# Optimization experiments

Hardware: AMD Instinct MI355X
Metric: run time of the kernel (lower is better)

## Reference

```python
import jax, jax.numpy as jnp
import numpy as np

H = 256          # hidden_dim
K = 5            # num_mixtures
Z = 32           # latent_dim
A = 3            # action dim
B, T = 128, 512
IN = Z + A       # LSTM input features
MDN = K * (1 + 2 * Z)  # 325


def setup_inputs() -> dict:
    key = jax.random.key(0)
    ks = jax.random.split(key, 8)
    s_in = 1.0 / np.sqrt(IN)
    s_h = 1.0 / np.sqrt(H)
    return {
        "z_t": jax.random.normal(ks[0], (B, T, Z), jnp.float32),
        "a_t": jax.random.normal(ks[1], (B, T, A), jnp.float32),
        # LSTM params: fused gate kernels, gate order [i, f, g, o]
        "Wx": jax.random.normal(ks[2], (IN, 4 * H), jnp.float32) * s_in,
        "Wh": jax.random.normal(ks[3], (H, 4 * H), jnp.float32) * s_h,
        "b": jnp.zeros((4 * H,), jnp.float32),
        # MDN head Dense(325)
        "Wd": jax.random.normal(ks[4], (H, MDN), jnp.float32) * s_h,
        "bd": jnp.zeros((MDN,), jnp.float32),
    }


def _mdnrnn(z_t, a_t, Wx, Wh, b, Wd, bd):
    x = jnp.concatenate([z_t, a_t], axis=-1)          # (B,T,IN)
    # hoist the input projection out of the recurrence (same math)
    xproj = jnp.einsum("bti,ig->btg", x, Wx)          # (B,T,4H)
    xproj_t = jnp.swapaxes(xproj, 0, 1)               # (T,B,4H)
    bsz = x.shape[0]
    c0 = jnp.zeros((bsz, H), x.dtype)
    h0 = jnp.zeros((bsz, H), x.dtype)

    def step(carry, xp):
        c, h = carry
        gates = xp + h @ Wh + b                        # (B,4H)
        i, f, g, o = jnp.split(gates, 4, axis=-1)
        i = jax.nn.sigmoid(i)
        f = jax.nn.sigmoid(f)
        g = jnp.tanh(g)
        o = jax.nn.sigmoid(o)
        c = f * c + i * g
        h = o * jnp.tanh(c)
        return (c, h), h

    final_carry, hs = jax.lax.scan(step, (c0, h0), xproj_t)
    outputs = jnp.swapaxes(hs, 0, 1)                  # (B,T,H)

    mdn = outputs @ Wd + bd                           # (B,T,325)
    log_pi, mu, log_sigma = jnp.split(mdn, [K, K + K * Z * 2 // 2 + K * Z - K], axis=-1)
    # splits: [K, (1+Z)*K] -> log_pi (K), mu (K*Z), log_sigma (K*Z)
    log_pi, mu, log_sigma = mdn[..., :K], mdn[..., K:K + K * Z], mdn[..., K + K * Z:]
    bt = outputs.shape[:2]
    mu = mu.reshape(bt[0], bt[1], K, Z)
    log_sigma = log_sigma.reshape(bt[0], bt[1], K, Z)
    log_pi = jax.nn.log_softmax(log_pi, axis=-1)
    sigma = jnp.exp(log_sigma) + 1e-06
    return log_pi, mu, sigma, final_carry


def reference(z_t, a_t, Wx, Wh, b, Wd, bd):
    return _mdnrnn(z_t, a_t, Wx, Wh, b, Wd, bd)
```

## Files before the change

### kernel.cpp

```cpp
#include <hip/hip_runtime.h>
#include <hip/hip_bf16.h>
#include <math.h>

#define T_LEN 512
#define B_SZ  128
#define H_DIM 256
#define G_DIM 1024
#define IN_D  35
#define MDN_D 325
#define K_MIX 5

#define NSLICE 4
#define BG     2
#define NGRP   64

static constexpr long OFF_MU    = 327680L;
static constexpr long OFF_SIGMA = 10813440L;
static constexpr long OFF_C     = 21299200L;
static constexpr long OFF_H     = 21331968L;

static constexpr size_t WS_OUT = 0;
static constexpr size_t WS_HG  = 33554432;

typedef unsigned uint2v  __attribute__((ext_vector_type(2)));
typedef float    float2v __attribute__((ext_vector_type(2)));
typedef float    float4v __attribute__((ext_vector_type(4)));

__device__ __forceinline__ float fast_sigmoid(float x) { return 1.0f / (1.0f + __expf(-x)); }
__device__ __forceinline__ float fast_tanh(float x) {
    return 1.0f - 2.0f / (__expf(2.0f * x) + 1.0f);
}

__device__ __forceinline__ void pk_fma_lo(float2v& acc, float2v w, float2v h) {
    asm("v_pk_fma_f32 %0, %1, %2, %0 op_sel:[0,0,0] op_sel_hi:[1,0,1]"
        : "+v"(acc) : "v"(w), "v"(h));
}
__device__ __forceinline__ void pk_fma_hi(float2v& acc, float2v w, float2v h) {
    asm("v_pk_fma_f32 %0, %1, %2, %0 op_sel:[0,1,0] op_sel_hi:[1,1,1]"
        : "+v"(acc) : "v"(w), "v"(h));
}

__global__ __launch_bounds__(512, 1) void lstm6_kernel(
    const float* __restrict__ z_t, const float* __restrict__ a_t,
    const float* __restrict__ Wx,  const float* __restrict__ Wh,
    const float* __restrict__ bias,
    float* __restrict__ h_glb,
    __hip_bfloat16* __restrict__ outs,
    float* __restrict__ out_c, float* __restrict__ out_h)
{
    const int bid = blockIdx.x;
    const int gr  = bid & 63;
    const int s   = bid >> 6;
    const int tid = threadIdx.x;
    const int cg  = tid >> 2;
    const int kq  = tid & 3;
    const int lc0 = cg * 2;
    const int gate = lc0 >> 6;
    const int j0   = lc0 & 63;
    const int gcol0 = gate * 256 + s * 64 + j0;

    __shared__ __align__(16) float h_lds[BG][4][68];
    __shared__ __align__(16) float x_lds[BG][44];
    __shared__ __align__(16) float g_red[BG][256];

    for (int i = tid; i < BG * 4 * 68; i += 512) ((float*)h_lds)[i] = 0.0f;
    if (tid < BG * 9) { int b = tid / 9, k = tid - 9 * b; x_lds[b][35 + k] = 0.0f; }

    float2v W2[64];
    #pragma unroll
    for (int i = 0; i < 64; ++i) {
        const size_t r = (size_t)(kq * 64 + i) * G_DIM;
        W2[i].x = Wh[r + gcol0];
        W2[i].y = Wh[r + gcol0 + 1];
    }
    float2v X2[10];
    #pragma unroll
    for (int i = 0; i < 10; ++i) {
        int xk = kq * 10 + i;
        bool ok = (xk < IN_D);
        X2[i].x = ok ? Wx[(size_t)xk * G_DIM + gcol0]     : 0.0f;
        X2[i].y = ok ? Wx[(size_t)xk * G_DIM + gcol0 + 1] : 0.0f;
    }
    #pragma unroll
    for (int i = 0; i < 64; ++i) asm volatile("" : "+v"(W2[i]));
    #pragma unroll
    for (int i = 0; i < 10; ++i) asm volatile("" : "+v"(X2[i]));

    const int cb = tid >> 6;
    const int cj = tid & 63;
    const float bc0 = bias[0 * 256 + s * 64 + cj];
    const float bc1 = bias[1 * 256 + s * 64 + cj];
    const float bc2 = bias[2 * 256 + s * 64 + cj];
    const float bc3 = bias[3 * 256 + s * 64 + cj];
    float c_reg = 0.0f;

    const int q  = tid - 128;
    const int pb = (q >= 96) ? 1 : 0;
    const int pp = q - 96 * pb;
    const int pk0 = pp * 2;
    const int pkk = pk0 + ((pk0 >= s * 64) ? 64 : 0);

    const int batch0 = gr * BG;
    float* hg = h_glb + (size_t)gr * (2 * BG * H_DIM);

    if (tid >= 384 && tid < 448) {
        int qq = tid - 384, b = qq >> 5, k = qq & 31;
        x_lds[b][k] = z_t[((size_t)(batch0 + b) * T_LEN + 0) * 32 + k];
    } else if (tid >= 448 && tid < 448 + BG * 3) {
        int qq = tid - 448, b = (qq >= 3), k = qq - 3 * b;
        x_lds[b][32 + k] = a_t[((size_t)(batch0 + b) * T_LEN + 0) * 3 + k];
    }
    __syncthreads();

    for (int t = 0; t < T_LEN; ++t) {
        if (t > 0 && tid >= 128 && tid < 320) {
            const unsigned want = (unsigned)((t - 1) & 3);
            const float* ap = hg + ((t - 1) & 1) * (BG * H_DIM) + pb * H_DIM + pkk;
            uint2v u;
            do {
                asm volatile("global_load_dwordx2 %0, %1, off sc0 sc1\n\t"
                             "s_waitcnt vmcnt(0)"
                             : "=v"(u) : "v"(ap) : "memory");
            } while ((u.x & 3u) != want || (u.y & 3u) != want);
            float* dst = &h_lds[pb][pkk >> 6][pkk & 63];
            dst[0] = __uint_as_float(u.x);
            dst[1] = __uint_as_float(u.y);
        }
        __syncthreads();

        float2v acc0 = {0.0f, 0.0f}, acc1 = {0.0f, 0.0f};
        {
            const float4v* hp0 = (const float4v*)h_lds[0][kq];
            const float4v* hp1 = (const float4v*)h_lds[1][kq];
            #pragma unroll
            for (int i4 = 0; i4 < 16; ++i4) {
                float4v hv0 = hp0[i4];
                float4v hv1 = hp1[i4];
                float2v h0lo = __builtin_shufflevector(hv0, hv0, 0, 1);
                float2v h0hi = __builtin_shufflevector(hv0, hv0, 2, 3);
                float2v h1lo = __builtin_shufflevector(hv1, hv1, 0, 1);
                float2v h1hi = __builtin_shufflevector(hv1, hv1, 2, 3);
                pk_fma_lo(acc0, W2[4*i4+0], h0lo); pk_fma_lo(acc1, W2[4*i4+0], h1lo);
                pk_fma_hi(acc0, W2[4*i4+1], h0lo); pk_fma_hi(acc1, W2[4*i4+1], h1lo);
                pk_fma_lo(acc0, W2[4*i4+2], h0hi); pk_fma_lo(acc1, W2[4*i4+2], h1hi);
                pk_fma_hi(acc0, W2[4*i4+3], h0hi); pk_fma_hi(acc1, W2[4*i4+3], h1hi);
            }
            #pragma unroll
            for (int i = 0; i < 5; ++i) {
                float2v xv0 = *(const float2v*)&x_lds[0][kq * 10 + 2 * i];
                float2v xv1 = *(const float2v*)&x_lds[1][kq * 10 + 2 * i];
                pk_fma_lo(acc0, X2[2*i],   xv0); pk_fma_lo(acc1, X2[2*i],   xv1);
                pk_fma_hi(acc0, X2[2*i+1], xv0); pk_fma_hi(acc1, X2[2*i+1], xv1);
            }
        }
        float a00 = acc0.x, a01 = acc0.y, a10 = acc1.x, a11 = acc1.y;
        a00 += __shfl_xor(a00, 1, 64); a00 += __shfl_xor(a00, 2, 64);
        a01 += __shfl_xor(a01, 1, 64); a01 += __shfl_xor(a01, 2, 64);
        a10 += __shfl_xor(a10, 1, 64); a10 += __shfl_xor(a10, 2, 64);
        a11 += __shfl_xor(a11, 1, 64); a11 += __shfl_xor(a11, 2, 64);
        if (kq == 0) {
            g_red[0][lc0] = a00; g_red[0][lc0 + 1] = a01;
            g_red[1][lc0] = a10; g_red[1][lc0 + 1] = a11;
        }
        __syncthreads();

        if (tid < 128) {
            float gi = g_red[cb][      cj] + bc0;
            float gf = g_red[cb][ 64 + cj] + bc1;
            float gg = g_red[cb][128 + cj] + bc2;
            float go = g_red[cb][192 + cj] + bc3;
            float iv = fast_sigmoid(gi), fv = fast_sigmoid(gf), ov = fast_sigmoid(go);
            float gv = fast_tanh(gg);
            c_reg = fmaf(fv, c_reg, iv * gv);
            float hv = ov * fast_tanh(c_reg);
            unsigned u = (__float_as_uint(hv) & ~3u) | (unsigned)(t & 3);
            float* dst = hg + (t & 1) * (BG * H_DIM) + cb * H_DIM + s * 64 + cj;
            asm volatile("global_store_dword %0, %1, off sc0 sc1"
                         :: "v"(dst), "v"(u) : "memory");
            h_lds[cb][s][cj] = __uint_as_float(u);
            outs[((size_t)(batch0 + cb) * T_LEN + t) * H_DIM + s * 64 + cj] =
                __float2bfloat16(hv);
            if (t == T_LEN - 1) {
                out_c[(batch0 + cb) * H_DIM + s * 64 + cj] = c_reg;
                out_h[(batch0 + cb) * H_DIM + s * 64 + cj] = hv;
            }
        }
        if (t + 1 < T_LEN) {
            if (tid >= 384 && tid < 448) {
                int qq = tid - 384, b = qq >> 5, k = qq & 31;
                x_lds[b][k] = z_t[((size_t)(batch0 + b) * T_LEN + (t + 1)) * 32 + k];
            } else if (tid >= 448 && tid < 448 + BG * 3) {
                int qq = tid - 448, b = (qq >= 3), k = qq - 3 * b;
                x_lds[b][32 + k] = a_t[((size_t)(batch0 + b) * T_LEN + (t + 1)) * 3 + k];
            }
        }
    }
}

__global__ __launch_bounds__(256, 1) void mdn_kernel(
    const unsigned short* __restrict__ outputs, const float* __restrict__ Wd,
    const float* __restrict__ bd, float* __restrict__ out)
{
    __shared__ __align__(16) float hT[H_DIM * 16];
    __shared__ float lp[16][K_MIX];

    const int tid = threadIdx.x;
    const long row0 = (long)blockIdx.x * 16;

    for (int idx = tid; idx < H_DIM * 16; idx += 256) {
        int r = idx >> 8;
        int k = idx & (H_DIM - 1);
        unsigned int u = outputs[(row0 + r) * H_DIM + k];
        hT[k * 16 + r] = __uint_as_float(u << 16);
    }
    __syncthreads();

    const int  cA = tid;
    const int  cB = tid + 256;
    const bool vB = (cB < MDN_D);
    const float bA = bd[cA];
    const float bB = vB ? bd[cB] : 0.0f;
    float accA[16], accB[16];
    #pragma unroll
    for (int r = 0; r < 16; ++r) { accA[r] = bA; accB[r] = bB; }

    for (int k = 0; k < H_DIM; ++k) {
        float wA = Wd[(size_t)k * MDN_D + cA];
        float wB = vB ? Wd[(size_t)k * MDN_D + cB] : 0.0f;
        const float4* hp = (const float4*)(hT + k * 16);
        float4 h0 = hp[0], h1 = hp[1], h2 = hp[2], h3 = hp[3];
        float hr[16] = { h0.x,h0.y,h0.z,h0.w, h1.x,h1.y,h1.z,h1.w,
                         h2.x,h2.y,h2.z,h2.w, h3.x,h3.y,h3.z,h3.w };
        #pragma unroll
        for (int r = 0; r < 16; ++r) {
            accA[r] = fmaf(hr[r], wA, accA[r]);
            accB[r] = fmaf(hr[r], wB, accB[r]);
        }
    }

    float* out_mu = out + OFF_MU;
    float* out_sg = out + OFF_SIGMA;
    #pragma unroll
    for (int r = 0; r < 16; ++r) {
        long row = row0 + r;
        float v = accA[r];
        if (cA < K_MIX)            lp[r][cA] = v;
        else if (cA < K_MIX + 160) out_mu[row * 160 + (cA - K_MIX)] = v;
        else                       out_sg[row * 160 + (cA - 165)]   = __expf(v) + 1e-6f;
        if (vB)                    out_sg[row * 160 + (cB - 165)]   = __expf(accB[r]) + 1e-6f;
    }
    __syncthreads();

    if (tid < 16) {
        int r = tid;
        long row = row0 + r;
        float v0 = lp[r][0], v1 = lp[r][1], v2 = lp[r][2], v3 = lp[r][3], v4 = lp[r][4];
        float m = fmaxf(fmaxf(fmaxf(v0, v1), fmaxf(v2, v3)), v4);
        float sum = __expf(v0-m) + __expf(v1-m) + __expf(v2-m) + __expf(v3-m) + __expf(v4-m);
        float ls = m + __logf(sum);
        out[row*5 + 0] = v0 - ls;
        out[row*5 + 1] = v1 - ls;
        out[row*5 + 2] = v2 - ls;
        out[row*5 + 3] = v3 - ls;
        out[row*5 + 4] = v4 - ls;
    }
}

extern "C" void kernel_launch(void* const* d_in, const int* in_sizes, int n_in,
                              void* d_out, int out_size, void* d_ws, size_t ws_size,
                              hipStream_t stream)
{
    const float* z_t = (const float*)d_in[0];
    const float* a_t = (const float*)d_in[1];
    const float* Wx  = (const float*)d_in[2];
    const float* Wh  = (const float*)d_in[3];
    const float* b   = (const float*)d_in[4];
    const float* Wd  = (const float*)d_in[5];
    const float* bd  = (const float*)d_in[6];
    float* out = (float*)d_out;

    char* ws = (char*)d_ws;
    __hip_bfloat16* outs = (__hip_bfloat16*)(ws + WS_OUT);
    float* h_glb         = (float*)(ws + WS_HG);

    lstm6_kernel<<<NGRP * NSLICE, 512, 0, stream>>>(z_t, a_t, Wx, Wh, b,
                                                    h_glb, outs,
                                                    out + OFF_C, out + OFF_H);
    mdn_kernel<<<(B_SZ * T_LEN) / 16, 256, 0, stream>>>((const unsigned short*)outs,
                                                        Wd, bd, out);
}
```

Measured before the change: 1.192 ms.

## Remove per-step gate reduction barrier and double-buffer h/x LDS in LSTM

Each thread now owns two gate columns of the same hidden unit (i/g and f/o pairs across two lanes), so the gate nonlinearity and cell update happen in registers after a shuffle exchange, not in a separate 128-thread phase behind a shared reduction buffer. This removes one __syncthreads and the g_red LDS round trip per timestep. h and x LDS are double-buffered, the x input is prefetched one step ahead into a register, and the cross-block h polling is spread over 384 threads with single-dword loads issued two in flight. The cost is redundant activation math on every thread and more spin traffic on the global h buffer.

```diff
diff --git a/kernel.cpp b/kernel.cpp
--- a/kernel.cpp
+++ b/kernel.cpp
@@ -40,7 +40,7 @@
         : "+v"(acc) : "v"(w), "v"(h));
 }
 
-__global__ __launch_bounds__(512, 1) void lstm6_kernel(
+__global__ __launch_bounds__(512, 1) void lstm7_kernel(
     const float* __restrict__ z_t, const float* __restrict__ a_t,
     const float* __restrict__ Wx,  const float* __restrict__ Wh,
     const float* __restrict__ bias,
@@ -52,86 +52,96 @@
     const int gr  = bid & 63;
     const int s   = bid >> 6;
     const int tid = threadIdx.x;
-    const int cg  = tid >> 2;
     const int kq  = tid & 3;
-    const int lc0 = cg * 2;
-    const int gate = lc0 >> 6;
-    const int j0   = lc0 & 63;
-    const int gcol0 = gate * 256 + s * 64 + j0;
-
-    __shared__ __align__(16) float h_lds[BG][4][68];
-    __shared__ __align__(16) float x_lds[BG][44];
-    __shared__ __align__(16) float g_red[BG][256];
-
-    for (int i = tid; i < BG * 4 * 68; i += 512) ((float*)h_lds)[i] = 0.0f;
-    if (tid < BG * 9) { int b = tid / 9, k = tid - 9 * b; x_lds[b][35 + k] = 0.0f; }
+    const int u   = (tid >> 2) & 1;
+    const int j   = tid >> 3;
+    const int cu0 = u * 256 + s * 64 + j;
+    const int cu1 = (u + 2) * 256 + s * 64 + j;
+
+    __shared__ __align__(16) float h_lds[2][BG][4][68];
+    __shared__ __align__(16) float x_lds[2][BG][44];
+
+    for (int i = tid; i < 2 * BG * 4 * 68; i += 512) ((float*)h_lds)[i] = 0.0f;
+    if (tid < 2 * BG * 9) {
+        int buf = tid / 18, r = tid % 18, b = r / 9, k = 35 + r % 9;
+        x_lds[buf][b][k] = 0.0f;
+    }
 
     float2v W2[64];
     #pragma unroll
     for (int i = 0; i < 64; ++i) {
         const size_t r = (size_t)(kq * 64 + i) * G_DIM;
-        W2[i].x = Wh[r + gcol0];
-        W2[i].y = Wh[r + gcol0 + 1];
+        W2[i].x = Wh[r + cu0];
+        W2[i].y = Wh[r + cu1];
     }
     float2v X2[10];
     #pragma unroll
     for (int i = 0; i < 10; ++i) {
         int xk = kq * 10 + i;
         bool ok = (xk < IN_D);
-        X2[i].x = ok ? Wx[(size_t)xk * G_DIM + gcol0]     : 0.0f;
-        X2[i].y = ok ? Wx[(size_t)xk * G_DIM + gcol0 + 1] : 0.0f;
+        X2[i].x = ok ? Wx[(size_t)xk * G_DIM + cu0] : 0.0f;
+        X2[i].y = ok ? Wx[(size_t)xk * G_DIM + cu1] : 0.0f;
     }
     #pragma unroll
     for (int i = 0; i < 64; ++i) asm volatile("" : "+v"(W2[i]));
     #pragma unroll
     for (int i = 0; i < 10; ++i) asm volatile("" : "+v"(X2[i]));
 
-    const int cb = tid >> 6;
-    const int cj = tid & 63;
-    const float bc0 = bias[0 * 256 + s * 64 + cj];
-    const float bc1 = bias[1 * 256 + s * 64 + cj];
-    const float bc2 = bias[2 * 256 + s * 64 + cj];
-    const float bc3 = bias[3 * 256 + s * 64 + cj];
-    float c_reg = 0.0f;
-
-    const int q  = tid - 128;
-    const int pb = (q >= 96) ? 1 : 0;
-    const int pp = q - 96 * pb;
-    const int pk0 = pp * 2;
-    const int pkk = pk0 + ((pk0 >= s * 64) ? 64 : 0);
+    const float bci = bias[0 * 256 + s * 64 + j];
+    const float bcf = bias[1 * 256 + s * 64 + j];
+    const float bcg = bias[2 * 256 + s * 64 + j];
+    const float bco = bias[3 * 256 + s * 64 + j];
+    float c0 = 0.0f, c1 = 0.0f;
+
+    const int pb  = (tid >= 192) ? 1 : 0;
+    const int pp  = tid - 192 * pb;
+    const int pkk = pp + ((pp >= s * 64) ? 64 : 0);
+
+    const int  sq    = tid - 384;
+    const bool is_st = (sq >= 0 && sq < 2 * IN_D);
+    const int  sb    = (sq >= IN_D) ? 1 : 0;
+    const int  sk    = sq - IN_D * sb;
+    float xreg = 0.0f;
 
     const int batch0 = gr * BG;
     float* hg = h_glb + (size_t)gr * (2 * BG * H_DIM);
 
-    if (tid >= 384 && tid < 448) {
-        int qq = tid - 384, b = qq >> 5, k = qq & 31;
-        x_lds[b][k] = z_t[((size_t)(batch0 + b) * T_LEN + 0) * 32 + k];
-    } else if (tid >= 448 && tid < 448 + BG * 3) {
-        int qq = tid - 448, b = (qq >= 3), k = qq - 3 * b;
-        x_lds[b][32 + k] = a_t[((size_t)(batch0 + b) * T_LEN + 0) * 3 + k];
+    if (is_st) {
+        x_lds[0][sb][sk] = (sk < 32)
+            ? z_t[((size_t)(batch0 + sb) * T_LEN + 0) * 32 + sk]
+            : a_t[((size_t)(batch0 + sb) * T_LEN + 0) * 3 + (sk - 32)];
+        xreg = (sk < 32)
+            ? z_t[((size_t)(batch0 + sb) * T_LEN + 1) * 32 + sk]
+            : a_t[((size_t)(batch0 + sb) * T_LEN + 1) * 3 + (sk - 32)];
     }
     __syncthreads();
 
     for (int t = 0; t < T_LEN; ++t) {
-        if (t > 0 && tid >= 128 && tid < 320) {
+        if (t > 0 && tid < 384) {
             const unsigned want = (unsigned)((t - 1) & 3);
             const float* ap = hg + ((t - 1) & 1) * (BG * H_DIM) + pb * H_DIM + pkk;
-            uint2v u;
-            do {
-                asm volatile("global_load_dwordx2 %0, %1, off sc0 sc1\n\t"
-                             "s_waitcnt vmcnt(0)"
-                             : "=v"(u) : "v"(ap) : "memory");
-            } while ((u.x & 3u) != want || (u.y & 3u) != want);
-            float* dst = &h_lds[pb][pkk >> 6][pkk & 63];
-            dst[0] = __uint_as_float(u.x);
-            dst[1] = __uint_as_float(u.y);
+            unsigned v0, v1, got;
+            asm volatile("global_load_dword %0, %1, off sc0 sc1"
+                         : "=v"(v0) : "v"(ap) : "memory");
+            for (;;) {
+                asm volatile("global_load_dword %0, %1, off sc0 sc1"
+                             : "=v"(v1) : "v"(ap) : "memory");
+                asm volatile("s_waitcnt vmcnt(1)" : "+v"(v0) :: "memory");
+                if ((v0 & 3u) == want) { got = v0; break; }
+                asm volatile("global_load_dword %0, %1, off sc0 sc1"
+                             : "=v"(v0) : "v"(ap) : "memory");
+                asm volatile("s_waitcnt vmcnt(1)" : "+v"(v1) :: "memory");
+                if ((v1 & 3u) == want) { got = v1; break; }
+            }
+            asm volatile("s_waitcnt vmcnt(0)" ::: "memory");
+            h_lds[(t - 1) & 1][pb][pkk >> 6][pkk & 63] = __uint_as_float(got);
         }
         __syncthreads();
 
         float2v acc0 = {0.0f, 0.0f}, acc1 = {0.0f, 0.0f};
         {
-            const float4v* hp0 = (const float4v*)h_lds[0][kq];
-            const float4v* hp1 = (const float4v*)h_lds[1][kq];
+            const float4v* hp0 = (const float4v*)h_lds[(t + 1) & 1][0][kq];
+            const float4v* hp1 = (const float4v*)h_lds[(t + 1) & 1][1][kq];
             #pragma unroll
             for (int i4 = 0; i4 < 16; ++i4) {
                 float4v hv0 = hp0[i4];
@@ -147,52 +157,57 @@
             }
             #pragma unroll
             for (int i = 0; i < 5; ++i) {
-                float2v xv0 = *(const float2v*)&x_lds[0][kq * 10 + 2 * i];
-                float2v xv1 = *(const float2v*)&x_lds[1][kq * 10 + 2 * i];
+                float2v xv0 = *(const float2v*)&x_lds[t & 1][0][kq * 10 + 2 * i];
+                float2v xv1 = *(const float2v*)&x_lds[t & 1][1][kq * 10 + 2 * i];
                 pk_fma_lo(acc0, X2[2*i],   xv0); pk_fma_lo(acc1, X2[2*i],   xv1);
                 pk_fma_hi(acc0, X2[2*i+1], xv0); pk_fma_hi(acc1, X2[2*i+1], xv1);
             }
         }
-        float a00 = acc0.x, a01 = acc0.y, a10 = acc1.x, a11 = acc1.y;
+        float a00 = acc0.x, a01 = acc0.y;
+        float a10 = acc1.x, a11 = acc1.y;
         a00 += __shfl_xor(a00, 1, 64); a00 += __shfl_xor(a00, 2, 64);
         a01 += __shfl_xor(a01, 1, 64); a01 += __shfl_xor(a01, 2, 64);
         a10 += __shfl_xor(a10, 1, 64); a10 += __shfl_xor(a10, 2, 64);
         a11 += __shfl_xor(a11, 1, 64); a11 += __shfl_xor(a11, 2, 64);
+        float r00 = __shfl_xor(a00, 4, 64);
+        float r01 = __shfl_xor(a01, 4, 64);
+        float r10 = __shfl_xor(a10, 4, 64);
+        float r11 = __shfl_xor(a11, 4, 64);
+        float gi0 = (u ? r00 : a00) + bci, gf0 = (u ? a00 : r00) + bcf;
+        float gg0 = (u ? r01 : a01) + bcg, go0 = (u ? a01 : r01) + bco;
+        float gi1 = (u ? r10 : a10) + bci, gf1 = (u ? a10 : r10) + bcf;
+        float gg1 = (u ? r11 : a11) + bcg, go1 = (u ? a11 : r11) + bco;
+
+        float iv0 = fast_sigmoid(gi0), fv0 = fast_sigmoid(gf0), ov0 = fast_sigmoid(go0);
+        float gv0 = fast_tanh(gg0);
+        c0 = fmaf(fv0, c0, iv0 * gv0);
+        float hv0 = ov0 * fast_tanh(c0);
+        float iv1 = fast_sigmoid(gi1), fv1 = fast_sigmoid(gf1), ov1 = fast_sigmoid(go1);
+        float gv1 = fast_tanh(gg1);
+        c1 = fmaf(fv1, c1, iv1 * gv1);
+        float hv1 = ov1 * fast_tanh(c1);
+
         if (kq == 0) {
-            g_red[0][lc0] = a00; g_red[0][lc0 + 1] = a01;
-            g_red[1][lc0] = a10; g_red[1][lc0 + 1] = a11;
-        }
-        __syncthreads();
-
-        if (tid < 128) {
-            float gi = g_red[cb][      cj] + bc0;
-            float gf = g_red[cb][ 64 + cj] + bc1;
-            float gg = g_red[cb][128 + cj] + bc2;
-            float go = g_red[cb][192 + cj] + bc3;
-            float iv = fast_sigmoid(gi), fv = fast_sigmoid(gf), ov = fast_sigmoid(go);
-            float gv = fast_tanh(gg);
-            c_reg = fmaf(fv, c_reg, iv * gv);
-            float hv = ov * fast_tanh(c_reg);
-            unsigned u = (__float_as_uint(hv) & ~3u) | (unsigned)(t & 3);
-            float* dst = hg + (t & 1) * (BG * H_DIM) + cb * H_DIM + s * 64 + cj;
+            float hvu = u ? hv1 : hv0;
+            float cu  = u ? c1 : c0;
+            unsigned tu = (__float_as_uint(hvu) & ~3u) | (unsigned)(t & 3);
+            float* dst = hg + (t & 1) * (BG * H_DIM) + u * H_DIM + s * 64 + j;
             asm volatile("global_store_dword %0, %1, off sc0 sc1"
-                         :: "v"(dst), "v"(u) : "memory");
-            h_lds[cb][s][cj] = __uint_as_float(u);
-            outs[((size_t)(batch0 + cb) * T_LEN + t) * H_DIM + s * 64 + cj] =
-                __float2bfloat16(hv);
+                         :: "v"(dst), "v"(tu) : "memory");
+            h_lds[t & 1][u][s][j] = __uint_as_float(tu);
+            outs[((size_t)(batch0 + u) * T_LEN + t) * H_DIM + s * 64 + j] =
+                __float2bfloat16(hvu);
             if (t == T_LEN - 1) {
-                out_c[(batch0 + cb) * H_DIM + s * 64 + cj] = c_reg;
-                out_h[(batch0 + cb) * H_DIM + s * 64 + cj] = hv;
+                out_c[(batch0 + u) * H_DIM + s * 64 + j] = cu;
+                out_h[(batch0 + u) * H_DIM + s * 64 + j] = hvu;
             }
         }
-        if (t + 1 < T_LEN) {
-            if (tid >= 384 && tid < 448) {
-                int qq = tid - 384, b = qq >> 5, k = qq & 31;
-                x_lds[b][k] = z_t[((size_t)(batch0 + b) * T_LEN + (t + 1)) * 32 + k];
-            } else if (tid >= 448 && tid < 448 + BG * 3) {
-                int qq = tid - 448, b = (qq >= 3), k = qq - 3 * b;
-                x_lds[b][32 + k] = a_t[((size_t)(batch0 + b) * T_LEN + (t + 1)) * 3 + k];
-            }
+        if (is_st) {
+            x_lds[(t + 1) & 1][sb][sk] = xreg;
+            if (t + 2 < T_LEN)
+                xreg = (sk < 32)
+                    ? z_t[((size_t)(batch0 + sb) * T_LEN + (t + 2)) * 32 + sk]
+                    : a_t[((size_t)(batch0 + sb) * T_LEN + (t + 2)) * 3 + (sk - 32)];
         }
     }
 }
@@ -283,7 +298,7 @@
     __hip_bfloat16* outs = (__hip_bfloat16*)(ws + WS_OUT);
     float* h_glb         = (float*)(ws + WS_HG);
 
-    lstm6_kernel<<<NGRP * NSLICE, 512, 0, stream>>>(z_t, a_t, Wx, Wh, b,
+    lstm7_kernel<<<NGRP * NSLICE, 512, 0, stream>>>(z_t, a_t, Wx, Wh, b,
                                                     h_glb, outs,
                                                     out + OFF_C, out + OFF_H);
     mdn_kernel<<<(B_SZ * T_LEN) / 16, 256, 0, stream>>>((const unsigned short*)outs,
```

New measurement: 1.858 ms. +55.8%, slower.

## Restructure LSTM step to split K across waves and drop one barrier per step

Applied to the files above, without the earlier changes.

Each wave now owns a 64-row K-chunk of the recurrent weights, and each lane computes two gate columns for both batch rows. Partial sums go to double-buffered LDS and are reduced by the waves that own the hidden slice, which removes the shuffle reduction and one __syncthreads per timestep. Non-owner waves poll the global h exchange buffer directly into per-wave LDS. Owner waves use their locally produced h without a global round trip. Inputs x are prefetched into registers two steps ahead and double-buffered in LDS. The cost is a more intricate cross-wave protocol in which correctness depends on the double-buffer parity and the tag bits.

```diff
diff --git a/kernel.cpp b/kernel.cpp
--- a/kernel.cpp
+++ b/kernel.cpp
@@ -40,7 +40,7 @@
         : "+v"(acc) : "v"(w), "v"(h));
 }
 
-__global__ __launch_bounds__(512, 1) void lstm6_kernel(
+__global__ __launch_bounds__(512, 1) void lstm8_kernel(
     const float* __restrict__ z_t, const float* __restrict__ a_t,
     const float* __restrict__ Wx,  const float* __restrict__ Wh,
     const float* __restrict__ bias,
@@ -48,150 +48,179 @@
     __hip_bfloat16* __restrict__ outs,
     float* __restrict__ out_c, float* __restrict__ out_h)
 {
-    const int bid = blockIdx.x;
-    const int gr  = bid & 63;
-    const int s   = bid >> 6;
-    const int tid = threadIdx.x;
-    const int cg  = tid >> 2;
-    const int kq  = tid & 3;
-    const int lc0 = cg * 2;
-    const int gate = lc0 >> 6;
-    const int j0   = lc0 & 63;
-    const int gcol0 = gate * 256 + s * 64 + j0;
-
-    __shared__ __align__(16) float h_lds[BG][4][68];
-    __shared__ __align__(16) float x_lds[BG][44];
-    __shared__ __align__(16) float g_red[BG][256];
-
-    for (int i = tid; i < BG * 4 * 68; i += 512) ((float*)h_lds)[i] = 0.0f;
-    if (tid < BG * 9) { int b = tid / 9, k = tid - 9 * b; x_lds[b][35 + k] = 0.0f; }
+    const int bid  = blockIdx.x;
+    const int gr   = bid & 63;
+    const int s    = bid >> 6;
+    const int tid  = threadIdx.x;
+    const int w    = tid >> 6;
+    const int lane = tid & 63;
+    const int cw   = w >> 1;
+    const int uw   = w & 1;
+    const bool own = (cw == s);
+    const int P    = uw * 64 + lane;
+    const int q0   = 2 * P;
+    const int gc0  = (q0 >> 6) * 256 + s * 64 + (q0 & 63);
+    const int gc1  = ((q0 + 1) >> 6) * 256 + s * 64 + ((q0 + 1) & 63);
+
+    __shared__ __align__(16) float2v hbuf[8][64];
+    __shared__ __align__(16) float  hown[2][2][64][2];
+    __shared__ __align__(16) float4v part[2][4][2][64];
+    __shared__ __align__(16) float  x_lds[2][2][36];
+    __shared__ __align__(16) float  xown[2][2][2][36];
+
+    if (tid < 4) x_lds[tid >> 1][tid & 1][35] = 0.0f;
+    if (own && lane < 4) xown[uw][lane >> 1][lane & 1][35] = 0.0f;
 
     float2v W2[64];
     #pragma unroll
     for (int i = 0; i < 64; ++i) {
-        const size_t r = (size_t)(kq * 64 + i) * G_DIM;
-        W2[i].x = Wh[r + gcol0];
-        W2[i].y = Wh[r + gcol0 + 1];
-    }
-    float2v X2[10];
-    #pragma unroll
-    for (int i = 0; i < 10; ++i) {
-        int xk = kq * 10 + i;
+        const size_t r = (size_t)(cw * 64 + i) * G_DIM;
+        W2[i].x = Wh[r + gc0];
+        W2[i].y = Wh[r + gc1];
+    }
+    float2v X2[9];
+    #pragma unroll
+    for (int i = 0; i < 9; ++i) {
+        int xk = cw * 9 + i;
         bool ok = (xk < IN_D);
-        X2[i].x = ok ? Wx[(size_t)xk * G_DIM + gcol0]     : 0.0f;
-        X2[i].y = ok ? Wx[(size_t)xk * G_DIM + gcol0 + 1] : 0.0f;
+        X2[i].x = ok ? Wx[(size_t)xk * G_DIM + gc0] : 0.0f;
+        X2[i].y = ok ? Wx[(size_t)xk * G_DIM + gc1] : 0.0f;
     }
     #pragma unroll
     for (int i = 0; i < 64; ++i) asm volatile("" : "+v"(W2[i]));
     #pragma unroll
-    for (int i = 0; i < 10; ++i) asm volatile("" : "+v"(X2[i]));
-
-    const int cb = tid >> 6;
-    const int cj = tid & 63;
-    const float bc0 = bias[0 * 256 + s * 64 + cj];
-    const float bc1 = bias[1 * 256 + s * 64 + cj];
-    const float bc2 = bias[2 * 256 + s * 64 + cj];
-    const float bc3 = bias[3 * 256 + s * 64 + cj];
-    float c_reg = 0.0f;
-
-    const int q  = tid - 128;
-    const int pb = (q >= 96) ? 1 : 0;
-    const int pp = q - 96 * pb;
-    const int pk0 = pp * 2;
-    const int pkk = pk0 + ((pk0 >= s * 64) ? 64 : 0);
+    for (int i = 0; i < 9; ++i)  asm volatile("" : "+v"(X2[i]));
+
+    float bg0 = 0, bg1 = 0, bg2 = 0, bg3 = 0, cc0 = 0.0f, cc1 = 0.0f;
+    if (own) {
+        bg0 = bias[0 * 256 + s * 64 + lane];
+        bg1 = bias[1 * 256 + s * 64 + lane];
+        bg2 = bias[2 * 256 + s * 64 + lane];
+        bg3 = bias[3 * 256 + s * 64 + lane];
+    }
 
     const int batch0 = gr * BG;
-    float* hg = h_glb + (size_t)gr * (2 * BG * H_DIM);
-
-    if (tid >= 384 && tid < 448) {
-        int qq = tid - 384, b = qq >> 5, k = qq & 31;
-        x_lds[b][k] = z_t[((size_t)(batch0 + b) * T_LEN + 0) * 32 + k];
-    } else if (tid >= 448 && tid < 448 + BG * 3) {
-        int qq = tid - 448, b = (qq >= 3), k = qq - 3 * b;
-        x_lds[b][32 + k] = a_t[((size_t)(batch0 + b) * T_LEN + 0) * 3 + k];
+    float* hg = h_glb + (size_t)gr * 1024;
+
+    const bool is_st = own && (lane < IN_D);
+    float xr0 = 0.0f, xr1 = 0.0f;
+    if (is_st) {
+        const int k = lane;
+        const size_t r0 = (size_t)(batch0 + 0) * T_LEN;
+        const size_t r1 = (size_t)(batch0 + 1) * T_LEN;
+        float v00 = (k < 32) ? z_t[(r0 + 0) * 32 + k] : a_t[(r0 + 0) * 3 + (k - 32)];
+        float v01 = (k < 32) ? z_t[(r1 + 0) * 32 + k] : a_t[(r1 + 0) * 3 + (k - 32)];
+        xown[uw][0][0][k] = v00;
+        xown[uw][0][1][k] = v01;
+        if (uw == 0) { x_lds[0][0][k] = v00; x_lds[0][1][k] = v01; }
+        xr0 = (k < 32) ? z_t[(r0 + 1) * 32 + k] : a_t[(r0 + 1) * 3 + (k - 32)];
+        xr1 = (k < 32) ? z_t[(r1 + 1) * 32 + k] : a_t[(r1 + 1) * 3 + (k - 32)];
     }
     __syncthreads();
 
     for (int t = 0; t < T_LEN; ++t) {
-        if (t > 0 && tid >= 128 && tid < 320) {
-            const unsigned want = (unsigned)((t - 1) & 3);
-            const float* ap = hg + ((t - 1) & 1) * (BG * H_DIM) + pb * H_DIM + pkk;
-            uint2v u;
-            do {
-                asm volatile("global_load_dwordx2 %0, %1, off sc0 sc1\n\t"
-                             "s_waitcnt vmcnt(0)"
-                             : "=v"(u) : "v"(ap) : "memory");
-            } while ((u.x & 3u) != want || (u.y & 3u) != want);
-            float* dst = &h_lds[pb][pkk >> 6][pkk & 63];
-            dst[0] = __uint_as_float(u.x);
-            dst[1] = __uint_as_float(u.y);
+        float2v acc0 = {0.0f, 0.0f}, acc1 = {0.0f, 0.0f};
+        if (t > 0) {
+            if (!own) {
+                const unsigned want = (unsigned)((t - 1) & 3);
+                const float* ap = hg + ((t - 1) & 1) * 512 + (cw * 64 + lane) * 2;
+                uint2v u;
+                do {
+                    asm volatile("global_load_dwordx2 %0, %1, off sc0 sc1\n\t"
+                                 "s_waitcnt vmcnt(0)"
+                                 : "=v"(u) : "v"(ap) : "memory");
+                } while ((u.x & 3u) != want || (u.y & 3u) != want);
+                float2v hv; hv.x = __uint_as_float(u.x); hv.y = __uint_as_float(u.y);
+                hbuf[w][lane] = hv;
+            }
+            const float4v* hp = own ? (const float4v*)hown[uw][(t - 1) & 1]
+                                    : (const float4v*)hbuf[w];
+            #pragma unroll
+            for (int i2 = 0; i2 < 32; ++i2) {
+                float4v hv = hp[i2];
+                float2v lo = __builtin_shufflevector(hv, hv, 0, 1);
+                float2v hi = __builtin_shufflevector(hv, hv, 2, 3);
+                pk_fma_lo(acc0, W2[2*i2],     lo);
+                pk_fma_hi(acc1, W2[2*i2],     lo);
+                pk_fma_lo(acc0, W2[2*i2 + 1], hi);
+                pk_fma_hi(acc1, W2[2*i2 + 1], hi);
+            }
+        }
+        {
+            const float* xb0 = own ? &xown[uw][t & 1][0][cw * 9] : &x_lds[t & 1][0][cw * 9];
+            const float* xb1 = own ? &xown[uw][t & 1][1][cw * 9] : &x_lds[t & 1][1][cw * 9];
+            #pragma unroll
+            for (int i = 0; i < 9; ++i) {
+                float2v xx; xx.x = xb0[i]; xx.y = xb1[i];
+                pk_fma_lo(acc0, X2[i], xx);
+                pk_fma_hi(acc1, X2[i], xx);
+            }
+        }
+        {
+            float4v pv; pv.x = acc0.x; pv.y = acc0.y; pv.z = acc1.x; pv.w = acc1.y;
+            part[t & 1][cw][uw][lane] = pv;
         }
         __syncthreads();
 
-        float2v acc0 = {0.0f, 0.0f}, acc1 = {0.0f, 0.0f};
-        {
-            const float4v* hp0 = (const float4v*)h_lds[0][kq];
-            const float4v* hp1 = (const float4v*)h_lds[1][kq];
+        if (own) {
+            const int j = lane;
+            float gb[4][2];
             #pragma unroll
-            for (int i4 = 0; i4 < 16; ++i4) {
-                float4v hv0 = hp0[i4];
-                float4v hv1 = hp1[i4];
-                float2v h0lo = __builtin_shufflevector(hv0, hv0, 0, 1);
-                float2v h0hi = __builtin_shufflevector(hv0, hv0, 2, 3);
-                float2v h1lo = __builtin_shufflevector(hv1, hv1, 0, 1);
-                float2v h1hi = __builtin_shufflevector(hv1, hv1, 2, 3);
-                pk_fma_lo(acc0, W2[4*i4+0], h0lo); pk_fma_lo(acc1, W2[4*i4+0], h1lo);
-                pk_fma_hi(acc0, W2[4*i4+1], h0lo); pk_fma_hi(acc1, W2[4*i4+1], h1lo);
-                pk_fma_lo(acc0, W2[4*i4+2], h0hi); pk_fma_lo(acc1, W2[4*i4+2], h1hi);
-                pk_fma_hi(acc0, W2[4*i4+3], h0hi); pk_fma_hi(acc1, W2[4*i4+3], h1hi);
-            }
-            #pragma unroll
-            for (int i = 0; i < 5; ++i) {
-                float2v xv0 = *(const float2v*)&x_lds[0][kq * 10 + 2 * i];
-                float2v xv1 = *(const float2v*)&x_lds[1][kq * 10 + 2 * i];
-                pk_fma_lo(acc0, X2[2*i],   xv0); pk_fma_lo(acc1, X2[2*i],   xv1);
-                pk_fma_hi(acc0, X2[2*i+1], xv0); pk_fma_hi(acc1, X2[2*i+1], xv1);
-            }
-        }
-        float a00 = acc0.x, a01 = acc0.y, a10 = acc1.x, a11 = acc1.y;
-        a00 += __shfl_xor(a00, 1, 64); a00 += __shfl_xor(a00, 2, 64);
-        a01 += __shfl_xor(a01, 1, 64); a01 += __shfl_xor(a01, 2, 64);
-        a10 += __shfl_xor(a10, 1, 64); a10 += __shfl_xor(a10, 2, 64);
-        a11 += __shfl_xor(a11, 1, 64); a11 += __shfl_xor(a11, 2, 64);
-        if (kq == 0) {
-            g_red[0][lc0] = a00; g_red[0][lc0 + 1] = a01;
-            g_red[1][lc0] = a10; g_red[1][lc0 + 1] = a11;
-        }
-        __syncthreads();
-
-        if (tid < 128) {
-            float gi = g_red[cb][      cj] + bc0;
-            float gf = g_red[cb][ 64 + cj] + bc1;
-            float gg = g_red[cb][128 + cj] + bc2;
-            float go = g_red[cb][192 + cj] + bc3;
-            float iv = fast_sigmoid(gi), fv = fast_sigmoid(gf), ov = fast_sigmoid(go);
-            float gv = fast_tanh(gg);
-            c_reg = fmaf(fv, c_reg, iv * gv);
-            float hv = ov * fast_tanh(c_reg);
-            unsigned u = (__float_as_uint(hv) & ~3u) | (unsigned)(t & 3);
-            float* dst = hg + (t & 1) * (BG * H_DIM) + cb * H_DIM + s * 64 + cj;
+            for (int g = 0; g < 4; ++g) {
+                const int hu = g >> 1, pl = (g & 1) * 32 + (j >> 1), e = j & 1;
+                const float* p = (const float*)&part[t & 1][0][hu][pl] + e;
+                float s0 = 0.0f, s1 = 0.0f;
+                #pragma unroll
+                for (int c = 0; c < 4; ++c) {
+                    s0 += p[c * 512];
+                    s1 += p[c * 512 + 2];
+                }
+                gb[g][0] = s0; gb[g][1] = s1;
+            }
+            float i0 = fast_sigmoid(gb[0][0] + bg0), f0 = fast_sigmoid(gb[1][0] + bg1);
+            float g0 = fast_tanh(gb[2][0] + bg2),    o0 = fast_sigmoid(gb[3][0] + bg3);
+            cc0 = fmaf(f0, cc0, i0 * g0);
+            float h0 = o0 * fast_tanh(cc0);
+            float i1 = fast_sigmoid(gb[0][1] + bg0), f1 = fast_sigmoid(gb[1][1] + bg1);
+            float g1 = fast_tanh(gb[2][1] + bg2),    o1 = fast_sigmoid(gb[3][1] + bg3);
+            cc1 = fmaf(f1, cc1, i1 * g1);
+            float h1 = o1 * fast_tanh(cc1);
+
+            const unsigned tg = (unsigned)(t & 3);
+            const unsigned tu0 = (__float_as_uint(h0) & ~3u) | tg;
+            const unsigned tu1 = (__float_as_uint(h1) & ~3u) | tg;
+
+            if (is_st && t + 1 < T_LEN) {
+                xown[uw][(t + 1) & 1][0][lane] = xr0;
+                xown[uw][(t + 1) & 1][1][lane] = xr1;
+                if (uw == 0) {
+                    x_lds[(t + 1) & 1][0][lane] = xr0;
+                    x_lds[(t + 1) & 1][1][lane] = xr1;
+                }
+            }
+            asm volatile("s_waitcnt lgkmcnt(0)" ::: "memory");
+
+            const unsigned tuu = uw ? tu1 : tu0;
+            float* dst = hg + (t & 1) * 512 + (s * 64 + j) * 2 + uw;
             asm volatile("global_store_dword %0, %1, off sc0 sc1"
-                         :: "v"(dst), "v"(u) : "memory");
-            h_lds[cb][s][cj] = __uint_as_float(u);
-            outs[((size_t)(batch0 + cb) * T_LEN + t) * H_DIM + s * 64 + cj] =
-                __float2bfloat16(hv);
+                         :: "v"(dst), "v"(tuu) : "memory");
+
+            float2v hw; hw.x = __uint_as_float(tu0); hw.y = __uint_as_float(tu1);
+            *(float2v*)&hown[uw][t & 1][j][0] = hw;
+
+            const float hvu = uw ? h1 : h0;
+            outs[((size_t)(batch0 + uw) * T_LEN + t) * H_DIM + s * 64 + j] =
+                __float2bfloat16(hvu);
             if (t == T_LEN - 1) {
-                out_c[(batch0 + cb) * H_DIM + s * 64 + cj] = c_reg;
-                out_h[(batch0 + cb) * H_DIM + s * 64 + cj] = hv;
-            }
-        }
-        if (t + 1 < T_LEN) {
-            if (tid >= 384 && tid < 448) {
-                int qq = tid - 384, b = qq >> 5, k = qq & 31;
-                x_lds[b][k] = z_t[((size_t)(batch0 + b) * T_LEN + (t + 1)) * 32 + k];
-            } else if (tid >= 448 && tid < 448 + BG * 3) {
-                int qq = tid - 448, b = (qq >= 3), k = qq - 3 * b;
-                x_lds[b][32 + k] = a_t[((size_t)(batch0 + b) * T_LEN + (t + 1)) * 3 + k];
+                out_c[(batch0 + uw) * H_DIM + s * 64 + j] = uw ? cc1 : cc0;
+                out_h[(batch0 + uw) * H_DIM + s * 64 + j] = hvu;
+            }
+            if (is_st && t + 2 < T_LEN) {
+                const int k = lane;
+                const size_t r0 = (size_t)(batch0 + 0) * T_LEN;
+                const size_t r1 = (size_t)(batch0 + 1) * T_LEN;
+                xr0 = (k < 32) ? z_t[(r0 + t + 2) * 32 + k] : a_t[(r0 + t + 2) * 3 + (k - 32)];
+                xr1 = (k < 32) ? z_t[(r1 + t + 2) * 32 + k] : a_t[(r1 + t + 2) * 3 + (k - 32)];
             }
         }
     }
@@ -283,7 +312,7 @@
     __hip_bfloat16* outs = (__hip_bfloat16*)(ws + WS_OUT);
     float* h_glb         = (float*)(ws + WS_HG);
 
-    lstm6_kernel<<<NGRP * NSLICE, 512, 0, stream>>>(z_t, a_t, Wx, Wh, b,
+    lstm8_kernel<<<NGRP * NSLICE, 512, 0, stream>>>(z_t, a_t, Wx, Wh, b,
                                                     h_glb, outs,
                                                     out + OFF_C, out + OFF_H);
     mdn_kernel<<<(B_SZ * T_LEN) / 16, 256, 0, stream>>>((const unsigned short*)outs,
```

After: 1.375 ms. +15.3%, slower.

## Store recurrent h in LDS as bf16, pipeline spin polls, double-buffer x

Applied to the files above, without the earlier changes.

The recurrent hidden state in LDS is now kept as packed bf16. This halves LDS read traffic per step, at the cost of unpacking and rounding h before the matvec, which adds precision error that compounds through the recurrence. The cross-block spin-wait now keeps two global loads in flight instead of waiting on each one, to shorten polling latency. The x input buffer is double-buffered so the prefetch of the next timestep does not race with reads of the current one.

```diff
diff --git a/kernel.cpp b/kernel.cpp
--- a/kernel.cpp
+++ b/kernel.cpp
@@ -24,7 +24,6 @@
 
 typedef unsigned uint2v  __attribute__((ext_vector_type(2)));
 typedef float    float2v __attribute__((ext_vector_type(2)));
-typedef float    float4v __attribute__((ext_vector_type(4)));
 
 __device__ __forceinline__ float fast_sigmoid(float x) { return 1.0f / (1.0f + __expf(-x)); }
 __device__ __forceinline__ float fast_tanh(float x) {
@@ -40,7 +39,17 @@
         : "+v"(acc) : "v"(w), "v"(h));
 }
 
-__global__ __launch_bounds__(512, 1) void lstm6_kernel(
+__device__ __forceinline__ unsigned f2bf(unsigned u) {
+    return (u + 0x7FFFu + ((u >> 16) & 1u)) >> 16;
+}
+__device__ __forceinline__ float2v bf2pair(unsigned d) {
+    float2v r;
+    r.x = __uint_as_float(d << 16);
+    r.y = __uint_as_float(d & 0xFFFF0000u);
+    return r;
+}
+
+__global__ __launch_bounds__(512, 1) void lstm10_kernel(
     const float* __restrict__ z_t, const float* __restrict__ a_t,
     const float* __restrict__ Wx,  const float* __restrict__ Wh,
     const float* __restrict__ bias,
@@ -59,12 +68,15 @@
     const int j0   = lc0 & 63;
     const int gcol0 = gate * 256 + s * 64 + j0;
 
-    __shared__ __align__(16) float h_lds[BG][4][68];
-    __shared__ __align__(16) float x_lds[BG][44];
+    __shared__ __align__(16) unsigned short h_bf[BG][4][80];
+    __shared__ __align__(16) float x_lds[2][BG][44];
     __shared__ __align__(16) float g_red[BG][256];
 
-    for (int i = tid; i < BG * 4 * 68; i += 512) ((float*)h_lds)[i] = 0.0f;
-    if (tid < BG * 9) { int b = tid / 9, k = tid - 9 * b; x_lds[b][35 + k] = 0.0f; }
+    for (int i = tid; i < (BG * 4 * 80) / 2; i += 512) ((unsigned*)h_bf)[i] = 0u;
+    if (tid < 2 * BG * 9) {
+        int buf = tid / 18, r = tid % 18, b = r / 9, k = 35 + r % 9;
+        x_lds[buf][b][k] = 0.0f;
+    }
 
     float2v W2[64];
     #pragma unroll
@@ -105,10 +117,10 @@
 
     if (tid >= 384 && tid < 448) {
         int qq = tid - 384, b = qq >> 5, k = qq & 31;
-        x_lds[b][k] = z_t[((size_t)(batch0 + b) * T_LEN + 0) * 32 + k];
+        x_lds[0][b][k] = z_t[((size_t)(batch0 + b) * T_LEN + 0) * 32 + k];
     } else if (tid >= 448 && tid < 448 + BG * 3) {
         int qq = tid - 448, b = (qq >= 3), k = qq - 3 * b;
-        x_lds[b][32 + k] = a_t[((size_t)(batch0 + b) * T_LEN + 0) * 3 + k];
+        x_lds[0][b][32 + k] = a_t[((size_t)(batch0 + b) * T_LEN + 0) * 3 + k];
     }
     __syncthreads();
 
@@ -116,39 +128,47 @@
         if (t > 0 && tid >= 128 && tid < 320) {
             const unsigned want = (unsigned)((t - 1) & 3);
             const float* ap = hg + ((t - 1) & 1) * (BG * H_DIM) + pb * H_DIM + pkk;
-            uint2v u;
-            do {
-                asm volatile("global_load_dwordx2 %0, %1, off sc0 sc1\n\t"
-                             "s_waitcnt vmcnt(0)"
-                             : "=v"(u) : "v"(ap) : "memory");
-            } while ((u.x & 3u) != want || (u.y & 3u) != want);
-            float* dst = &h_lds[pb][pkk >> 6][pkk & 63];
-            dst[0] = __uint_as_float(u.x);
-            dst[1] = __uint_as_float(u.y);
+            uint2v u0, u1, got;
+            asm volatile("global_load_dwordx2 %0, %1, off sc0 sc1"
+                         : "=v"(u0) : "v"(ap) : "memory");
+            for (;;) {
+                asm volatile("global_load_dwordx2 %0, %1, off sc0 sc1"
+                             : "=v"(u1) : "v"(ap) : "memory");
+                asm volatile("s_waitcnt vmcnt(1)" : "+v"(u0) :: "memory");
+                if ((u0.x & 3u) == want && (u0.y & 3u) == want) { got = u0; break; }
+                asm volatile("global_load_dwordx2 %0, %1, off sc0 sc1"
+                             : "=v"(u0) : "v"(ap) : "memory");
+                asm volatile("s_waitcnt vmcnt(1)" : "+v"(u1) :: "memory");
+                if ((u1.x & 3u) == want && (u1.y & 3u) == want) { got = u1; break; }
+            }
+            asm volatile("s_waitcnt vmcnt(0)" ::: "memory");
+            unsigned packed = f2bf(got.x) | (f2bf(got.y) << 16);
+            *(unsigned*)&h_bf[pb][pkk >> 6][pkk & 63] = packed;
         }
         __syncthreads();
 
         float2v acc0 = {0.0f, 0.0f}, acc1 = {0.0f, 0.0f};
         {
-            const float4v* hp0 = (const float4v*)h_lds[0][kq];
-            const float4v* hp1 = (const float4v*)h_lds[1][kq];
+            const uint4* hq0 = (const uint4*)&h_bf[0][kq][0];
+            const uint4* hq1 = (const uint4*)&h_bf[1][kq][0];
             #pragma unroll
-            for (int i4 = 0; i4 < 16; ++i4) {
-                float4v hv0 = hp0[i4];
-                float4v hv1 = hp1[i4];
-                float2v h0lo = __builtin_shufflevector(hv0, hv0, 0, 1);
-                float2v h0hi = __builtin_shufflevector(hv0, hv0, 2, 3);
-                float2v h1lo = __builtin_shufflevector(hv1, hv1, 0, 1);
-                float2v h1hi = __builtin_shufflevector(hv1, hv1, 2, 3);
-                pk_fma_lo(acc0, W2[4*i4+0], h0lo); pk_fma_lo(acc1, W2[4*i4+0], h1lo);
-                pk_fma_hi(acc0, W2[4*i4+1], h0lo); pk_fma_hi(acc1, W2[4*i4+1], h1lo);
-                pk_fma_lo(acc0, W2[4*i4+2], h0hi); pk_fma_lo(acc1, W2[4*i4+2], h1hi);
-                pk_fma_hi(acc0, W2[4*i4+3], h0hi); pk_fma_hi(acc1, W2[4*i4+3], h1hi);
+            for (int i8 = 0; i8 < 8; ++i8) {
+                uint4 d0 = hq0[i8];
+                uint4 d1 = hq1[i8];
+                float2v p;
+                p = bf2pair(d0.x); pk_fma_lo(acc0, W2[8*i8+0], p); pk_fma_hi(acc0, W2[8*i8+1], p);
+                p = bf2pair(d0.y); pk_fma_lo(acc0, W2[8*i8+2], p); pk_fma_hi(acc0, W2[8*i8+3], p);
+                p = bf2pair(d0.z); pk_fma_lo(acc0, W2[8*i8+4], p); pk_fma_hi(acc0, W2[8*i8+5], p);
+                p = bf2pair(d0.w); pk_fma_lo(acc0, W2[8*i8+6], p); pk_fma_hi(acc0, W2[8*i8+7], p);
+                p = bf2pair(d1.x); pk_fma_lo(acc1, W2[8*i8+0], p); pk_fma_hi(acc1, W2[8*i8+1], p);
+                p = bf2pair(d1.y); pk_fma_lo(acc1, W2[8*i8+2], p); pk_fma_hi(acc1, W2[8*i8+3], p);
+                p = bf2pair(d1.z); pk_fma_lo(acc1, W2[8*i8+4], p); pk_fma_hi(acc1, W2[8*i8+5], p);
+                p = bf2pair(d1.w); pk_fma_lo(acc1, W2[8*i8+6], p); pk_fma_hi(acc1, W2[8*i8+7], p);
             }
             #pragma unroll
             for (int i = 0; i < 5; ++i) {
-                float2v xv0 = *(const float2v*)&x_lds[0][kq * 10 + 2 * i];
-                float2v xv1 = *(const float2v*)&x_lds[1][kq * 10 + 2 * i];
+                float2v xv0 = *(const float2v*)&x_lds[t & 1][0][kq * 10 + 2 * i];
+                float2v xv1 = *(const float2v*)&x_lds[t & 1][1][kq * 10 + 2 * i];
                 pk_fma_lo(acc0, X2[2*i],   xv0); pk_fma_lo(acc1, X2[2*i],   xv1);
                 pk_fma_hi(acc0, X2[2*i+1], xv0); pk_fma_hi(acc1, X2[2*i+1], xv1);
             }
@@ -177,7 +197,7 @@
             float* dst = hg + (t & 1) * (BG * H_DIM) + cb * H_DIM + s * 64 + cj;
             asm volatile("global_store_dword %0, %1, off sc0 sc1"
                          :: "v"(dst), "v"(u) : "memory");
-            h_lds[cb][s][cj] = __uint_as_float(u);
+            h_bf[cb][s][cj] = (unsigned short)f2bf(u);
             outs[((size_t)(batch0 + cb) * T_LEN + t) * H_DIM + s * 64 + cj] =
                 __float2bfloat16(hv);
             if (t == T_LEN - 1) {
@@ -188,10 +208,12 @@
         if (t + 1 < T_LEN) {
             if (tid >= 384 && tid < 448) {
                 int qq = tid - 384, b = qq >> 5, k = qq & 31;
-                x_lds[b][k] = z_t[((size_t)(batch0 + b) * T_LEN + (t + 1)) * 32 + k];
+                x_lds[(t + 1) & 1][b][k] =
+                    z_t[((size_t)(batch0 + b) * T_LEN + (t + 1)) * 32 + k];
             } else if (tid >= 448 && tid < 448 + BG * 3) {
                 int qq = tid - 448, b = (qq >= 3), k = qq - 3 * b;
-                x_lds[b][32 + k] = a_t[((size_t)(batch0 + b) * T_LEN + (t + 1)) * 3 + k];
+                x_lds[(t + 1) & 1][b][32 + k] =
+                    a_t[((size_t)(batch0 + b) * T_LEN + (t + 1)) * 3 + k];
             }
         }
     }
@@ -283,9 +305,9 @@
     __hip_bfloat16* outs = (__hip_bfloat16*)(ws + WS_OUT);
     float* h_glb         = (float*)(ws + WS_HG);
 
-    lstm6_kernel<<<NGRP * NSLICE, 512, 0, stream>>>(z_t, a_t, Wx, Wh, b,
-                                                    h_glb, outs,
-                                                    out + OFF_C, out + OFF_H);
+    lstm10_kernel<<<NGRP * NSLICE, 512, 0, stream>>>(z_t, a_t, Wx, Wh, b,
+                                                     h_glb, outs,
+                                                     out + OFF_C, out + OFF_H);
     mdn_kernel<<<(B_SZ * T_LEN) / 16, 256, 0, stream>>>((const unsigned short*)outs,
                                                         Wd, bd, out);
 }
```

Measured after the change: 1.407 ms. 18.0% more time.
